# Performance work log

Hardware: AMD Instinct MI355X
Metric: run time of the kernel (lower is better)

The kernel has to match this reference:

```python
import jax, jax.numpy as jnp
import numpy as np

NEG_INF = -1e9


def setup_inputs() -> dict:
    key = jax.random.key(0)
    k1, k2, k3, k4 = jax.random.split(key, 4)
    N, F_in, F_out = 8192, 512, 256
    features = jax.random.normal(k1, (N, F_in), dtype=jnp.float32)
    adj = jax.random.randint(k2, (N, N), 0, 2).astype(jnp.float32)
    W = jax.random.normal(k3, (F_in, F_out), dtype=jnp.float32) * 0.05
    a = jax.random.normal(k4, (2 * F_out,), dtype=jnp.float32) * 0.05
    return {"features": features, "adj": adj, "W": W, "a": a}


def reference(features, adj, W, a):
    # h = W @ features  -> [N, F_out]
    h = features @ W
    F_out = h.shape[1]
    a_src, a_dst = a[:F_out], a[F_out:]
    # a^T [h_i ; h_j] decomposes into per-node dot products (same math as
    # the concat+linear in the original, without the [N,N,2F] intermediate).
    e = jax.nn.leaky_relu((h @ a_src)[:, None] + (h @ a_dst)[None, :],
                          negative_slope=0.01)  # [N, N]
    masked_e = e + NEG_INF * (1.0 - adj)
    attention = jax.nn.softmax(masked_e, axis=1)  # row-wise over neighbors j
    output = attention @ h  # [N, F_out]
    return output, attention
```

## Files before the change

### kernel.cpp

```cpp
#include <hip/hip_runtime.h>
#include <hip/hip_bf16.h>

#define N 8192
#define FIN 512
#define FOUT 256

typedef __attribute__((ext_vector_type(8))) short bf16x8;
typedef __attribute__((ext_vector_type(4))) float f32x4;

__device__ __forceinline__ unsigned short f2bf(float x) {
  unsigned int u = __float_as_uint(x);
  return (unsigned short)((u + 0x7FFFu + ((u >> 16) & 1u)) >> 16);
}

__device__ __forceinline__ void load_lds16(const void* g, void* l) {
  __builtin_amdgcn_global_load_lds(
      (const __attribute__((address_space(1))) void*)g,
      (__attribute__((address_space(3))) void*)l, 16, 0, 0);
}

__global__ __launch_bounds__(256) void gat_k1_gemm_h(
    const float* __restrict__ A, const float* __restrict__ W,
    float* __restrict__ h, unsigned short* __restrict__ hT) {
  __shared__ __align__(16) float As[16][68];
  __shared__ __align__(16) float Bs[16][64];
  const int tid = threadIdx.x;
  const int tx = tid & 15, ty = tid >> 4;
  const int nb = blockIdx.x * 64, mb = blockIdx.y * 64;
  float acc[4][4] = {};
  for (int k0 = 0; k0 < FIN; k0 += 16) {
#pragma unroll
    for (int i = 0; i < 4; ++i) {
      int e = tid + 256 * i;
      int m = e >> 4, k = e & 15;
      As[k][m] = A[(size_t)(mb + m) * FIN + k0 + k];
      int n2 = e & 63, k2 = e >> 6;
      Bs[k2][n2] = W[(size_t)(k0 + k2) * FOUT + nb + n2];
    }
    __syncthreads();
#pragma unroll
    for (int k = 0; k < 16; ++k) {
      float4 av = *reinterpret_cast<const float4*>(&As[k][ty * 4]);
      float4 bv = *reinterpret_cast<const float4*>(&Bs[k][tx * 4]);
      float aa[4] = {av.x, av.y, av.z, av.w};
      float bb[4] = {bv.x, bv.y, bv.z, bv.w};
#pragma unroll
      for (int i = 0; i < 4; ++i)
#pragma unroll
        for (int j = 0; j < 4; ++j) acc[i][j] = fmaf(aa[i], bb[j], acc[i][j]);
    }
    __syncthreads();
  }
#pragma unroll
  for (int i = 0; i < 4; ++i) {
    int m = mb + ty * 4 + i;
#pragma unroll
    for (int j = 0; j < 4; ++j) {
      int n = nb + tx * 4 + j;
      h[(size_t)m * FOUT + n] = acc[i][j];
      hT[(size_t)n * N + m] = f2bf(acc[i][j]);
    }
  }
}

__global__ __launch_bounds__(256) void gat_k2_hshd(
    const float* __restrict__ h, const float* __restrict__ a,
    float* __restrict__ hs, float* __restrict__ hd) {
  const int wid = threadIdx.x >> 6;
  const int lane = threadIdx.x & 63;
  const int row = blockIdx.x * 4 + wid;
  float ps = 0.f, pd = 0.f;
#pragma unroll
  for (int i = 0; i < 4; ++i) {
    int c = lane + 64 * i;
    float v = h[(size_t)row * FOUT + c];
    ps += v * a[c];
    pd += v * a[FOUT + c];
  }
#pragma unroll
  for (int off = 32; off >= 1; off >>= 1) {
    ps += __shfl_down(ps, off);
    pd += __shfl_down(pd, off);
  }
  if (lane == 0) {
    hs[row] = ps;
    hd[row] = pd;
  }
}

__global__ __launch_bounds__(1024, 4) void gat_fused(
    const float* __restrict__ adj, const float* __restrict__ hs,
    const float* __restrict__ hd, const unsigned short* __restrict__ hT,
    float* __restrict__ att, float* __restrict__ C) {
  __shared__ __align__(16) float hd_s[N];
  __shared__ __align__(16) unsigned short As[2][32 * 64];
  __shared__ __align__(16) unsigned short Bs[2][256 * 64];

  const int tid = threadIdx.x;
  const int lane = tid & 63;
  const int w = tid >> 6;
  const int wm = w >> 3, wn = w & 7;
  const int g = lane >> 4, rsel = lane & 15;
  const int row0 = blockIdx.x * 32;
  const int r = tid >> 5;
  const int c = tid & 31;

#pragma unroll
  for (int i = 0; i < 2; ++i) {
    int j = tid * 8 + i * 4;
    *reinterpret_cast<float4*>(&hd_s[j]) =
        *reinterpret_cast<const float4*>(&hd[j]);
  }
  const float hsv = hs[row0 + r];
  __syncthreads();

  unsigned int bits[8];
  float s = 0.f;
  const float* arow = adj + (size_t)(row0 + r) * N + c * 2;
#pragma unroll
  for (int to = 0; to < 8; ++to) {
    unsigned int wb = 0;
#pragma unroll 4
    for (int qi = 0; qi < 16; ++qi) {
      int q = to * 16 + qi;
      float2 a2 = *reinterpret_cast<const float2*>(arow + q * 64);
      float2 h2 = *reinterpret_cast<const float2*>(&hd_s[q * 64 + c * 2]);
      float x0 = hsv + h2.x, x1 = hsv + h2.y;
      float l0 = fmaxf(x0, 0.01f * x0);
      float l1 = fmaxf(x1, 0.01f * x1);
      unsigned int b0 = (a2.x != 0.f) ? 1u : 0u;
      unsigned int b1 = (a2.y != 0.f) ? 1u : 0u;
      s += (b0 ? __expf(l0) : 0.f) + (b1 ? __expf(l1) : 0.f);
      wb |= (b0 | (b1 << 1)) << (qi * 2);
    }
    bits[to] = wb;
  }
#pragma unroll
  for (int off = 16; off >= 1; off >>= 1) s += __shfl_xor(s, off);
  const float inv = 1.f / s;

  const unsigned short* bsrc0;
  const unsigned short* bsrc1;
  int bofs0, bofs1;
  {
    int s0 = tid, n0 = s0 >> 3, k0 = s0 & 7;
    bsrc0 = hT + (size_t)n0 * N + (k0 ^ (n0 & 7)) * 8;
    bofs0 = s0 * 16;
    int s1 = tid + 1024, n1 = s1 >> 3, k1 = s1 & 7;
    bsrc1 = hT + (size_t)n1 * N + (k1 ^ (n1 & 7)) * 8;
    bofs1 = s1 * 16;
  }
  float* aout = att + (size_t)(row0 + r) * N + c * 2;
  const int awbyte = r * 128 + ((c * 4) ^ ((r & 7) << 4));
  const int fr = wm * 16 + rsel;
  const int abase = fr * 128;
  const int asw = (fr & 7) << 4;

  f32x4 acc[2] = {};

#pragma unroll
  for (int to = 0; to < 8; ++to) {
    unsigned int wb = bits[to];
    for (int ti = 0; ti < 16; ++ti) {
      const int t = to * 16 + ti;
      const int kb = t * 64;
      char* Bw = reinterpret_cast<char*>(Bs[t & 1]);
      load_lds16(bsrc0 + kb, Bw + bofs0);
      load_lds16(bsrc1 + kb, Bw + bofs1);
      {
        float2 h2 = *reinterpret_cast<const float2*>(&hd_s[kb + c * 2]);
        unsigned int duo = wb >> (ti * 2);
        float x0 = hsv + h2.x, x1 = hsv + h2.y;
        float l0 = fmaxf(x0, 0.01f * x0);
        float l1 = fmaxf(x1, 0.01f * x1);
        float p0 = (duo & 1) ? __expf(l0) * inv : 0.f;
        float p1 = (duo & 2) ? __expf(l1) * inv : 0.f;
        *reinterpret_cast<float2*>(aout + kb) = make_float2(p0, p1);
        unsigned int pk = (unsigned)f2bf(p0) | ((unsigned)f2bf(p1) << 16);
        *reinterpret_cast<unsigned int*>(
            reinterpret_cast<char*>(As[t & 1]) + awbyte) = pk;
      }
      if (t > 0) {
        const char* Ar = reinterpret_cast<const char*>(As[(t & 1) ^ 1]);
        const char* Br = reinterpret_cast<const char*>(Bs[(t & 1) ^ 1]);
#pragma unroll
        for (int ks = 0; ks < 2; ++ks) {
          bf16x8 af = *reinterpret_cast<const bf16x8*>(
              Ar + abase + ((ks * 64 + g * 16) ^ asw));
#pragma unroll
          for (int f = 0; f < 2; ++f) {
            int n = wn * 32 + f * 16 + rsel;
            bf16x8 bg = *reinterpret_cast<const bf16x8*>(
                Br + n * 128 + ((ks * 64 + g * 16) ^ ((n & 7) << 4)));
            acc[f] = __builtin_amdgcn_mfma_f32_16x16x32_bf16(af, bg, acc[f],
                                                             0, 0, 0);
          }
        }
      }
      __syncthreads();
    }
  }
  {
    const char* Ar = reinterpret_cast<const char*>(As[1]);
    const char* Br = reinterpret_cast<const char*>(Bs[1]);
#pragma unroll
    for (int ks = 0; ks < 2; ++ks) {
      bf16x8 af = *reinterpret_cast<const bf16x8*>(
          Ar + abase + ((ks * 64 + g * 16) ^ asw));
#pragma unroll
      for (int f = 0; f < 2; ++f) {
        int n = wn * 32 + f * 16 + rsel;
        bf16x8 bg = *reinterpret_cast<const bf16x8*>(
            Br + n * 128 + ((ks * 64 + g * 16) ^ ((n & 7) << 4)));
        acc[f] = __builtin_amdgcn_mfma_f32_16x16x32_bf16(af, bg, acc[f],
                                                         0, 0, 0);
      }
    }
  }
#pragma unroll
  for (int f = 0; f < 2; ++f)
#pragma unroll
    for (int rr = 0; rr < 4; ++rr) {
      int row = row0 + wm * 16 + g * 4 + rr;
      int col = wn * 32 + f * 16 + rsel;
      C[(size_t)row * FOUT + col] = acc[f][rr];
    }
}

extern "C" void kernel_launch(void* const* d_in, const int* in_sizes, int n_in,
                              void* d_out, int out_size, void* d_ws, size_t ws_size,
                              hipStream_t stream) {
  const float* features = (const float*)d_in[0];
  const float* adj = (const float*)d_in[1];
  const float* W = (const float*)d_in[2];
  const float* a = (const float*)d_in[3];

  float* out = (float*)d_out;
  float* att = out + (size_t)N * FOUT;

  char* ws = (char*)d_ws;
  float* h = (float*)ws;
  unsigned short* hT = (unsigned short*)(ws + (size_t)N * FOUT * 4);
  float* hs = (float*)(ws + (size_t)N * FOUT * 4 + (size_t)N * FOUT * 2);
  float* hd = hs + N;

  hipLaunchKernelGGL(gat_k1_gemm_h, dim3(FOUT / 64, N / 64), dim3(256), 0,
                     stream, features, W, h, hT);
  hipLaunchKernelGGL(gat_k2_hshd, dim3(N / 4), dim3(256), 0, stream, h, a, hs,
                     hd);
  hipLaunchKernelGGL(gat_fused, dim3(N / 32), dim3(1024), 0, stream, adj, hs,
                     hd, hT, att, out);
}
```

Measured before the change: 274.5 us.

## Load hT B-fragments directly into registers and shrink fused block to 16 rows

The fused attention kernel now uses 512-thread blocks covering 16 rows instead of 1024 threads over 32 rows. The LDS staging of the hT tile via global_load_lds is replaced by per-wave register double-buffered loads of the B fragments straight from global memory. Probability work is split between two half-groups that alternate tiles, and adjacency and attention accesses are widened to float4. This removes the large B LDS buffer and its barrier traffic, at the cost of each wave re-reading hT from global/L2 with no sharing across waves and twice as many blocks each re-reading all of hT.

```diff
diff --git a/kernel.cpp b/kernel.cpp
--- a/kernel.cpp
+++ b/kernel.cpp
@@ -13,10 +13,10 @@
   return (unsigned short)((u + 0x7FFFu + ((u >> 16) & 1u)) >> 16);
 }
 
-__device__ __forceinline__ void load_lds16(const void* g, void* l) {
-  __builtin_amdgcn_global_load_lds(
-      (const __attribute__((address_space(1))) void*)g,
-      (__attribute__((address_space(3))) void*)l, 16, 0, 0);
+__device__ __forceinline__ void tile_barrier() {
+  asm volatile("s_waitcnt lgkmcnt(0)" ::: "memory");
+  __builtin_amdgcn_s_barrier();
+  __builtin_amdgcn_sched_barrier(0);
 }
 
 __global__ __launch_bounds__(256) void gat_k1_gemm_h(
@@ -88,26 +88,25 @@
   }
 }
 
-__global__ __launch_bounds__(1024, 4) void gat_fused(
+__global__ __launch_bounds__(512, 4) void gat_fused(
     const float* __restrict__ adj, const float* __restrict__ hs,
     const float* __restrict__ hd, const unsigned short* __restrict__ hT,
     float* __restrict__ att, float* __restrict__ C) {
   __shared__ __align__(16) float hd_s[N];
-  __shared__ __align__(16) unsigned short As[2][32 * 64];
-  __shared__ __align__(16) unsigned short Bs[2][256 * 64];
+  __shared__ __align__(16) unsigned short As[2][16 * 64];
 
   const int tid = threadIdx.x;
   const int lane = tid & 63;
-  const int w = tid >> 6;
-  const int wm = w >> 3, wn = w & 7;
+  const int wn = tid >> 6;
   const int g = lane >> 4, rsel = lane & 15;
-  const int row0 = blockIdx.x * 32;
+  const int row0 = blockIdx.x * 16;
   const int r = tid >> 5;
-  const int c = tid & 31;
-
-#pragma unroll
-  for (int i = 0; i < 2; ++i) {
-    int j = tid * 8 + i * 4;
+  const int par = (tid >> 4) & 1;
+  const int slot = tid & 15;
+
+#pragma unroll
+  for (int i = 0; i < 4; ++i) {
+    int j = (tid + 512 * i) * 4;
     *reinterpret_cast<float4*>(&hd_s[j]) =
         *reinterpret_cast<const float4*>(&hd[j]);
   }
@@ -116,22 +115,27 @@
 
   unsigned int bits[8];
   float s = 0.f;
-  const float* arow = adj + (size_t)(row0 + r) * N + c * 2;
+  const int hb = par * 64 + slot * 4;
+  const float* arow = adj + (size_t)(row0 + r) * N + hb;
 #pragma unroll
   for (int to = 0; to < 8; ++to) {
     unsigned int wb = 0;
-#pragma unroll 4
-    for (int qi = 0; qi < 16; ++qi) {
-      int q = to * 16 + qi;
-      float2 a2 = *reinterpret_cast<const float2*>(arow + q * 64);
-      float2 h2 = *reinterpret_cast<const float2*>(&hd_s[q * 64 + c * 2]);
-      float x0 = hsv + h2.x, x1 = hsv + h2.y;
-      float l0 = fmaxf(x0, 0.01f * x0);
-      float l1 = fmaxf(x1, 0.01f * x1);
-      unsigned int b0 = (a2.x != 0.f) ? 1u : 0u;
-      unsigned int b1 = (a2.y != 0.f) ? 1u : 0u;
-      s += (b0 ? __expf(l0) : 0.f) + (b1 ? __expf(l1) : 0.f);
-      wb |= (b0 | (b1 << 1)) << (qi * 2);
+#pragma unroll
+    for (int qi = 0; qi < 8; ++qi) {
+      int q = to * 8 + qi;
+      float4 a4 = *reinterpret_cast<const float4*>(arow + q * 128);
+      float4 h4 = *reinterpret_cast<const float4*>(&hd_s[q * 128 + hb]);
+      float x0 = hsv + h4.x, x1 = hsv + h4.y;
+      float x2 = hsv + h4.z, x3 = hsv + h4.w;
+      float l0 = fmaxf(x0, 0.01f * x0), l1 = fmaxf(x1, 0.01f * x1);
+      float l2 = fmaxf(x2, 0.01f * x2), l3 = fmaxf(x3, 0.01f * x3);
+      unsigned int b0 = (a4.x != 0.f) ? 1u : 0u;
+      unsigned int b1 = (a4.y != 0.f) ? 1u : 0u;
+      unsigned int b2 = (a4.z != 0.f) ? 1u : 0u;
+      unsigned int b3 = (a4.w != 0.f) ? 1u : 0u;
+      s += (b0 ? __expf(l0) : 0.f) + (b1 ? __expf(l1) : 0.f) +
+           (b2 ? __expf(l2) : 0.f) + (b3 ? __expf(l3) : 0.f);
+      wb |= (b0 | (b1 << 1) | (b2 << 2) | (b3 << 3)) << (qi * 4);
     }
     bits[to] = wb;
   }
@@ -139,81 +143,96 @@
   for (int off = 16; off >= 1; off >>= 1) s += __shfl_xor(s, off);
   const float inv = 1.f / s;
 
-  const unsigned short* bsrc0;
-  const unsigned short* bsrc1;
-  int bofs0, bofs1;
-  {
-    int s0 = tid, n0 = s0 >> 3, k0 = s0 & 7;
-    bsrc0 = hT + (size_t)n0 * N + (k0 ^ (n0 & 7)) * 8;
-    bofs0 = s0 * 16;
-    int s1 = tid + 1024, n1 = s1 >> 3, k1 = s1 & 7;
-    bsrc1 = hT + (size_t)n1 * N + (k1 ^ (n1 & 7)) * 8;
-    bofs1 = s1 * 16;
-  }
-  float* aout = att + (size_t)(row0 + r) * N + c * 2;
-  const int awbyte = r * 128 + ((c * 4) ^ ((r & 7) << 4));
-  const int fr = wm * 16 + rsel;
-  const int abase = fr * 128;
-  const int asw = (fr & 7) << 4;
+  const unsigned short* bp[2][2];
+#pragma unroll
+  for (int ks = 0; ks < 2; ++ks)
+#pragma unroll
+    for (int f = 0; f < 2; ++f)
+      bp[ks][f] = hT + (size_t)(wn * 32 + f * 16 + rsel) * N + ks * 32 + g * 8;
+
+  float* aoutb = att + (size_t)(row0 + r) * N + slot * 4;
+  const int awbyte = r * 128 + (((slot >> 1) ^ (r & 7)) << 4) + (slot & 1) * 8;
+  const int abase = rsel * 128;
+  const int asw = (rsel & 7) << 4;
 
   f32x4 acc[2] = {};
+  bf16x8 Bc00, Bc01, Bc10, Bc11, Bn00, Bn01, Bn10, Bn11;
+  Bc00 = *reinterpret_cast<const bf16x8*>(bp[0][0]);
+  Bc01 = *reinterpret_cast<const bf16x8*>(bp[0][1]);
+  Bc10 = *reinterpret_cast<const bf16x8*>(bp[1][0]);
+  Bc11 = *reinterpret_cast<const bf16x8*>(bp[1][1]);
 
 #pragma unroll
   for (int to = 0; to < 8; ++to) {
-    unsigned int wb = bits[to];
-    for (int ti = 0; ti < 16; ++ti) {
-      const int t = to * 16 + ti;
-      const int kb = t * 64;
-      char* Bw = reinterpret_cast<char*>(Bs[t & 1]);
-      load_lds16(bsrc0 + kb, Bw + bofs0);
-      load_lds16(bsrc1 + kb, Bw + bofs1);
-      {
-        float2 h2 = *reinterpret_cast<const float2*>(&hd_s[kb + c * 2]);
-        unsigned int duo = wb >> (ti * 2);
-        float x0 = hsv + h2.x, x1 = hsv + h2.y;
-        float l0 = fmaxf(x0, 0.01f * x0);
-        float l1 = fmaxf(x1, 0.01f * x1);
-        float p0 = (duo & 1) ? __expf(l0) * inv : 0.f;
-        float p1 = (duo & 2) ? __expf(l1) * inv : 0.f;
-        *reinterpret_cast<float2*>(aout + kb) = make_float2(p0, p1);
-        unsigned int pk = (unsigned)f2bf(p0) | ((unsigned)f2bf(p1) << 16);
-        *reinterpret_cast<unsigned int*>(
-            reinterpret_cast<char*>(As[t & 1]) + awbyte) = pk;
-      }
-      if (t > 0) {
-        const char* Ar = reinterpret_cast<const char*>(As[(t & 1) ^ 1]);
-        const char* Br = reinterpret_cast<const char*>(Bs[(t & 1) ^ 1]);
-#pragma unroll
-        for (int ks = 0; ks < 2; ++ks) {
-          bf16x8 af = *reinterpret_cast<const bf16x8*>(
-              Ar + abase + ((ks * 64 + g * 16) ^ asw));
-#pragma unroll
-          for (int f = 0; f < 2; ++f) {
-            int n = wn * 32 + f * 16 + rsel;
-            bf16x8 bg = *reinterpret_cast<const bf16x8*>(
-                Br + n * 128 + ((ks * 64 + g * 16) ^ ((n & 7) << 4)));
-            acc[f] = __builtin_amdgcn_mfma_f32_16x16x32_bf16(af, bg, acc[f],
-                                                             0, 0, 0);
-          }
-        }
-      }
-      __syncthreads();
-    }
-  }
-  {
-    const char* Ar = reinterpret_cast<const char*>(As[1]);
-    const char* Br = reinterpret_cast<const char*>(Bs[1]);
-#pragma unroll
-    for (int ks = 0; ks < 2; ++ks) {
-      bf16x8 af = *reinterpret_cast<const bf16x8*>(
-          Ar + abase + ((ks * 64 + g * 16) ^ asw));
-#pragma unroll
-      for (int f = 0; f < 2; ++f) {
-        int n = wn * 32 + f * 16 + rsel;
-        bf16x8 bg = *reinterpret_cast<const bf16x8*>(
-            Br + n * 128 + ((ks * 64 + g * 16) ^ ((n & 7) << 4)));
-        acc[f] = __builtin_amdgcn_mfma_f32_16x16x32_bf16(af, bg, acc[f],
-                                                         0, 0, 0);
+    const unsigned int wb = bits[to];
+    for (int tp = 0; tp < 8; ++tp) {
+      const int t = to * 16 + tp * 2;
+      {
+        const int kb = (t + 1) * 64;
+        Bn00 = *reinterpret_cast<const bf16x8*>(bp[0][0] + kb);
+        Bn01 = *reinterpret_cast<const bf16x8*>(bp[0][1] + kb);
+        Bn10 = *reinterpret_cast<const bf16x8*>(bp[1][0] + kb);
+        Bn11 = *reinterpret_cast<const bf16x8*>(bp[1][1] + kb);
+      }
+      if (par == 0) {
+        unsigned int nib = wb >> (tp * 4);
+        float4 h4 = *reinterpret_cast<const float4*>(&hd_s[t * 64 + slot * 4]);
+        float x0 = hsv + h4.x, x1 = hsv + h4.y;
+        float x2 = hsv + h4.z, x3 = hsv + h4.w;
+        float p0 = (nib & 1) ? __expf(fmaxf(x0, 0.01f * x0)) * inv : 0.f;
+        float p1 = (nib & 2) ? __expf(fmaxf(x1, 0.01f * x1)) * inv : 0.f;
+        float p2 = (nib & 4) ? __expf(fmaxf(x2, 0.01f * x2)) * inv : 0.f;
+        float p3 = (nib & 8) ? __expf(fmaxf(x3, 0.01f * x3)) * inv : 0.f;
+        *reinterpret_cast<float4*>(aoutb + t * 64) =
+            make_float4(p0, p1, p2, p3);
+        uint2 pk;
+        pk.x = (unsigned)f2bf(p0) | ((unsigned)f2bf(p1) << 16);
+        pk.y = (unsigned)f2bf(p2) | ((unsigned)f2bf(p3) << 16);
+        *reinterpret_cast<uint2*>(reinterpret_cast<char*>(As[0]) + awbyte) = pk;
+      }
+      tile_barrier();
+      {
+        const char* Ac = reinterpret_cast<const char*>(As[0]);
+        bf16x8 af0 = *reinterpret_cast<const bf16x8*>(Ac + abase + ((g * 16) ^ asw));
+        acc[0] = __builtin_amdgcn_mfma_f32_16x16x32_bf16(af0, Bc00, acc[0], 0, 0, 0);
+        acc[1] = __builtin_amdgcn_mfma_f32_16x16x32_bf16(af0, Bc01, acc[1], 0, 0, 0);
+        bf16x8 af1 = *reinterpret_cast<const bf16x8*>(Ac + abase + ((64 + g * 16) ^ asw));
+        acc[0] = __builtin_amdgcn_mfma_f32_16x16x32_bf16(af1, Bc10, acc[0], 0, 0, 0);
+        acc[1] = __builtin_amdgcn_mfma_f32_16x16x32_bf16(af1, Bc11, acc[1], 0, 0, 0);
+      }
+      {
+        const int kb = ((t + 2) & 127) * 64;
+        Bc00 = *reinterpret_cast<const bf16x8*>(bp[0][0] + kb);
+        Bc01 = *reinterpret_cast<const bf16x8*>(bp[0][1] + kb);
+        Bc10 = *reinterpret_cast<const bf16x8*>(bp[1][0] + kb);
+        Bc11 = *reinterpret_cast<const bf16x8*>(bp[1][1] + kb);
+      }
+      if (par == 1) {
+        unsigned int nib = wb >> (tp * 4);
+        float4 h4 =
+            *reinterpret_cast<const float4*>(&hd_s[(t + 1) * 64 + slot * 4]);
+        float x0 = hsv + h4.x, x1 = hsv + h4.y;
+        float x2 = hsv + h4.z, x3 = hsv + h4.w;
+        float p0 = (nib & 1) ? __expf(fmaxf(x0, 0.01f * x0)) * inv : 0.f;
+        float p1 = (nib & 2) ? __expf(fmaxf(x1, 0.01f * x1)) * inv : 0.f;
+        float p2 = (nib & 4) ? __expf(fmaxf(x2, 0.01f * x2)) * inv : 0.f;
+        float p3 = (nib & 8) ? __expf(fmaxf(x3, 0.01f * x3)) * inv : 0.f;
+        *reinterpret_cast<float4*>(aoutb + (t + 1) * 64) =
+            make_float4(p0, p1, p2, p3);
+        uint2 pk;
+        pk.x = (unsigned)f2bf(p0) | ((unsigned)f2bf(p1) << 16);
+        pk.y = (unsigned)f2bf(p2) | ((unsigned)f2bf(p3) << 16);
+        *reinterpret_cast<uint2*>(reinterpret_cast<char*>(As[1]) + awbyte) = pk;
+      }
+      tile_barrier();
+      {
+        const char* Ac = reinterpret_cast<const char*>(As[1]);
+        bf16x8 af0 = *reinterpret_cast<const bf16x8*>(Ac + abase + ((g * 16) ^ asw));
+        acc[0] = __builtin_amdgcn_mfma_f32_16x16x32_bf16(af0, Bn00, acc[0], 0, 0, 0);
+        acc[1] = __builtin_amdgcn_mfma_f32_16x16x32_bf16(af0, Bn01, acc[1], 0, 0, 0);
+        bf16x8 af1 = *reinterpret_cast<const bf16x8*>(Ac + abase + ((64 + g * 16) ^ asw));
+        acc[0] = __builtin_amdgcn_mfma_f32_16x16x32_bf16(af1, Bn10, acc[0], 0, 0, 0);
+        acc[1] = __builtin_amdgcn_mfma_f32_16x16x32_bf16(af1, Bn11, acc[1], 0, 0, 0);
       }
     }
   }
@@ -221,7 +240,7 @@
   for (int f = 0; f < 2; ++f)
 #pragma unroll
     for (int rr = 0; rr < 4; ++rr) {
-      int row = row0 + wm * 16 + g * 4 + rr;
+      int row = row0 + g * 4 + rr;
       int col = wn * 32 + f * 16 + rsel;
       C[(size_t)row * FOUT + col] = acc[f][rr];
     }
@@ -248,6 +267,6 @@
                      stream, features, W, h, hT);
   hipLaunchKernelGGL(gat_k2_hshd, dim3(N / 4), dim3(256), 0, stream, h, a, hs,
                      hd);
-  hipLaunchKernelGGL(gat_fused, dim3(N / 32), dim3(1024), 0, stream, adj, hs,
+  hipLaunchKernelGGL(gat_fused, dim3(N / 16), dim3(512), 0, stream, adj, hs,
                      hd, hT, att, out);
 }
```

Result: slower. 341.4 us (+24.4%).
